# Kernel optimization log

Hardware: AMD Instinct MI355X
Metric: run time of the kernel (lower is better)

The kernel has to match this reference:

```python
import jax, jax.numpy as jnp
import numpy as np

PC_RANGE = [-51.2, -51.2, -5.0, 51.2, 51.2, 3.0]
VOXEL = [0.1, 0.1, 0.2]
OSF = 8
NUM_PRIOR = 100
C = 256
BN_EPS = 1e-5
LN_EPS = 1e-5


def _conv(x, w, pad):
    # x: [B,C,H,W], w: [O,I,kh,kw]
    return jax.lax.conv_general_dilated(
        x, w, window_strides=(1, 1), padding=[(pad, pad), (pad, pad)],
        dimension_numbers=('NCHW', 'OIHW', 'NCHW'))


def _bn(x, g, b, m, v):
    scale = (g / jnp.sqrt(v + BN_EPS))[None, :, None, None]
    return (x - m[None, :, None, None]) * scale + b[None, :, None, None]


def setup_inputs() -> dict:
    key = jax.random.key(0)
    ks = jax.random.split(key, 24)
    s3 = 1.0 / np.sqrt(C * 9)
    s1 = 1.0 / np.sqrt(C)
    inp = {
        'bev_feat': jax.random.normal(ks[0], (4, C, 128, 128), jnp.float32),
        'template_anchor': jax.random.normal(ks[1], (4, 900, 11), jnp.float32),
        # shared_conv: 3x3 conv (no bias) + BN(eval) + ReLU
        'shared_w': jax.random.normal(ks[2], (C, C, 3, 3), jnp.float32) * s3,
        'bn1_g': jax.random.normal(ks[3], (C,), jnp.float32) * 0.1 + 1.0,
        'bn1_b': jax.random.normal(ks[4], (C,), jnp.float32) * 0.1,
        'bn1_m': jax.random.normal(ks[5], (C,), jnp.float32) * 0.1,
        'bn1_v': jax.random.uniform(ks[6], (C,), jnp.float32) + 0.5,
        # objectness: 3x3 conv (no bias) + BN + ReLU + 1x1 conv (bias=-2)
        'obj_w1': jax.random.normal(ks[7], (C, C, 3, 3), jnp.float32) * s3,
        'bn2_g': jax.random.normal(ks[8], (C,), jnp.float32) * 0.1 + 1.0,
        'bn2_b': jax.random.normal(ks[9], (C,), jnp.float32) * 0.1,
        'bn2_m': jax.random.normal(ks[10], (C,), jnp.float32) * 0.1,
        'bn2_v': jax.random.uniform(ks[11], (C,), jnp.float32) + 0.5,
        'obj_w2': jax.random.normal(ks[12], (1, C, 1, 1), jnp.float32) * s1,
        'obj_b2': jnp.full((1,), -2.0, jnp.float32),
        # feat_proj: Linear + LN + ReLU + Linear
        'fp_w1': jax.random.normal(ks[13], (C, C), jnp.float32) * s1,
        'fp_b1': jax.random.normal(ks[14], (C,), jnp.float32) * 0.01,
        'ln_g': jnp.ones((C,), jnp.float32),
        'ln_b': jnp.zeros((C,), jnp.float32),
        'fp_w2': jax.random.normal(ks[15], (C, C), jnp.float32) * s1,
        'fp_b2': jax.random.normal(ks[16], (C,), jnp.float32) * 0.01,
        # geometry heads (1x1 convs, bias init 0)
        'z_w': jax.random.normal(ks[17], (1, C, 1, 1), jnp.float32) * s1,
        'z_b': jnp.zeros((1,), jnp.float32),
        'dim_w': jax.random.normal(ks[18], (3, C, 1, 1), jnp.float32) * s1,
        'dim_b': jnp.zeros((3,), jnp.float32),
        'yaw_w': jax.random.normal(ks[19], (2, C, 1, 1), jnp.float32) * s1,
        'yaw_b': jnp.zeros((2,), jnp.float32),
        'vel_w': jax.random.normal(ks[20], (2, C, 1, 1), jnp.float32) * s1,
        'vel_b': jnp.zeros((2,), jnp.float32),
    }
    return inp


def _forward(bev_feat, template_anchor, shared_w, bn1_g, bn1_b, bn1_m, bn1_v,
             obj_w1, bn2_g, bn2_b, bn2_m, bn2_v, obj_w2, obj_b2,
             fp_w1, fp_b1, ln_g, ln_b, fp_w2, fp_b2,
             z_w, z_b, dim_w, dim_b, yaw_w, yaw_b, vel_w, vel_b):
    B, Cc, H, W = bev_feat.shape
    # shared_conv
    feat = jax.nn.relu(_bn(_conv(bev_feat, shared_w, 1), bn1_g, bn1_b, bn1_m, bn1_v))
    # objectness heatmap
    h = jax.nn.relu(_bn(_conv(feat, obj_w1, 1), bn2_g, bn2_b, bn2_m, bn2_v))
    heatmap = jax.nn.sigmoid(_conv(h, obj_w2, 0) + obj_b2[None, :, None, None])
    score = heatmap.reshape(B, H * W)
    K = min(NUM_PRIOR, H * W, template_anchor.shape[1])
    topk_score, topk_inds = jax.lax.top_k(score, K)  # [B,K]
    ys = topk_inds // W
    xs = topk_inds % W
    # gather BEV features at topk locations: [B,K,C]
    feat_flat = feat.reshape(B, Cc, H * W).transpose(0, 2, 1)
    gathered = jnp.take_along_axis(feat_flat, topk_inds[:, :, None], axis=1)
    # feat_proj: Linear + LN + ReLU + Linear
    x = gathered @ fp_w1.T + fp_b1
    mu = jnp.mean(x, axis=-1, keepdims=True)
    var = jnp.mean((x - mu) ** 2, axis=-1, keepdims=True)
    x = (x - mu) / jnp.sqrt(var + LN_EPS) * ln_g + ln_b
    x = jax.nn.relu(x)
    prior_feature = x @ fp_w2.T + fp_b2
    prior_feature = prior_feature * (1.0 + topk_score[:, :, None])
    # geometry heads (1x1 convs == linear on gathered features)
    z_pred = gathered @ z_w[:, :, 0, 0].T + z_b      # [B,K,1]
    dim_pred = gathered @ dim_w[:, :, 0, 0].T + dim_b  # [B,K,3]
    yaw_pred = gathered @ yaw_w[:, :, 0, 0].T + yaw_b  # [B,K,2]
    vel_pred = gathered @ vel_w[:, :, 0, 0].T + vel_b  # [B,K,2]
    # anchor update
    pa = template_anchor[:, :K, :]
    x_metric = (xs.astype(pa.dtype) + 0.5) * (VOXEL[0] * OSF) + PC_RANGE[0]
    y_metric = (ys.astype(pa.dtype) + 0.5) * (VOXEL[1] * OSF) + PC_RANGE[1]
    z_new = pa[..., 2] + 0.5 * z_pred[..., 0]
    dims_new = pa[..., 3:6] + 0.2 * jnp.clip(dim_pred, -1.0, 1.0)
    yaw = jnp.tanh(yaw_pred)
    nrm = jnp.maximum(jnp.sqrt(jnp.sum(yaw * yaw, axis=-1, keepdims=True)), 1e-6)
    yaw_new = 0.7 * pa[..., 6:8] + 0.3 * (yaw / nrm)
    vel_new = pa[..., 8:10] + 0.2 * jnp.clip(vel_pred, -2.0, 2.0)
    prior_anchor = jnp.concatenate([
        x_metric[..., None], y_metric[..., None], z_new[..., None],
        dims_new, yaw_new, vel_new, pa[..., 10:]], axis=-1)
    return prior_feature, prior_anchor, topk_score


def reference(bev_feat, template_anchor, shared_w, bn1_g, bn1_b, bn1_m, bn1_v,
              obj_w1, bn2_g, bn2_b, bn2_m, bn2_v, obj_w2, obj_b2,
              fp_w1, fp_b1, ln_g, ln_b, fp_w2, fp_b2,
              z_w, z_b, dim_w, dim_b, yaw_w, yaw_b, vel_w, vel_b):
    return _forward(bev_feat, template_anchor, shared_w, bn1_g, bn1_b, bn1_m, bn1_v,
                    obj_w1, bn2_g, bn2_b, bn2_m, bn2_v, obj_w2, obj_b2,
                    fp_w1, fp_b1, ln_g, ln_b, fp_w2, fp_b2,
                    z_w, z_b, dim_w, dim_b, yaw_w, yaw_b, vel_w, vel_b)
```

## Files before the change

### kernel.cpp

```cpp
#include <hip/hip_runtime.h>
#include <math.h>


typedef __attribute__((ext_vector_type(8))) short bf16x8;
typedef __attribute__((ext_vector_type(4))) float f32x4;

#define HW 16384
#define WPITCH 130
#define CCAP 192
#define PSTR 28
#define WSO_XN    0ULL
#define WSO_FEATB 34078720ULL
#define WSO_WP1   68157440ULL
#define WSO_WP2   69337088ULL
#define WSO_BNP   70516736ULL
#define WSO_LOG   70521856ULL
#define WSO_CAND  70784000ULL
#define WSO_CNT   70787072ULL
#define WSO_EXL   70787136ULL
#define WSO_TIDX  70790208ULL
#define WSO_TLOG  70791808ULL
#define WSO_W1N   70793408ULL
#define WSO_W2N   73152704ULL
#define WSO_PBUF  WSO_XN

__device__ __forceinline__ float bf2f(short s) {
  return __uint_as_float(((unsigned)(unsigned short)s) << 16);
}
__device__ __forceinline__ short f2bf(float f) {
  unsigned u = __float_as_uint(f);
  u += 0x7fffu + ((u >> 16) & 1u);
  return (short)(u >> 16);
}
__device__ __forceinline__ void gll16(const void* g, void* l) {
  __builtin_amdgcn_global_load_lds(
      (const __attribute__((address_space(1))) void*)g,
      (__attribute__((address_space(3))) void*)l, 16, 0, 0);
}

__global__ void wprep(const float* __restrict__ src, short* __restrict__ wp,
                      float* __restrict__ wn) {
  int i = blockIdx.x * 256 + threadIdx.x;
  float v = src[i];
  int k = i % 9;
  int r = i / 9;
  int ci = r & 255;
  int co = r >> 8;
  wp[(k * 256 + co) * 256 + ci] = f2bf(v);
  wn[(ci * 9 + k) * 256 + co] = v;
}

__global__ void bnprep(const float* g1, const float* b1, const float* m1,
                       const float* v1, const float* g2, const float* b2,
                       const float* m2, const float* v2, const float* w2,
                       float* __restrict__ out) {
  int c = threadIdx.x;
  float s1 = g1[c] / sqrtf(v1[c] + 1e-5f);
  out[c] = s1;
  out[256 + c] = b1[c] - m1[c] * s1;
  float s2 = g2[c] / sqrtf(v2[c] + 1e-5f);
  out[512 + c] = s2;
  out[768 + c] = b2[c] - m2[c] * s2;
  out[1024 + c] = w2[c];
}

__global__ void padzero(short* __restrict__ xn, short* __restrict__ featb) {
  int i = blockIdx.x * 256 + threadIdx.x;
  int c = i & 255;
  int r = i >> 8;
  int nh = r >> 1;
  int side = r & 1;
  size_t off = ((size_t)nh * WPITCH + (side ? 129 : 0)) * 256 + c;
  xn[off] = 0;
  featb[off] = 0;
}

__global__ void loginit(float* __restrict__ logits, const float* __restrict__ b2) {
  logits[blockIdx.x * 256 + threadIdx.x] = b2[0];
}

__global__ __launch_bounds__(256) void nchw2nhwc(const float* __restrict__ in,
                                                 short* __restrict__ out) {
  __shared__ short tl[64 * 66];
  int n = blockIdx.z, c0 = blockIdx.y * 64, s0 = blockIdx.x * 64;
  int sl = threadIdx.x & 63, cl = threadIdx.x >> 6;
  for (int p = 0; p < 16; ++p) {
    int c = cl + p * 4;
    tl[c * 66 + sl] = f2bf(in[(((size_t)(n * 256 + c0 + c)) << 14) + s0 + sl]);
  }
  __syncthreads();
  int co = threadIdx.x & 63, so = threadIdx.x >> 6;
  for (int p = 0; p < 16; ++p) {
    int S = s0 + so + p * 4;
    int h = S >> 7, w = S & 127;
    out[(((size_t)(n * 128 + h)) * WPITCH + w + 1) * 256 + c0 + co] =
        tl[co * 66 + (so + p * 4)];
  }
}

template <int OUT_LOGITS>
__global__ __launch_bounds__(256) void conv3x3(const short* __restrict__ inp,
                                               const short* __restrict__ wp,
                                               const float* __restrict__ scale,
                                               const float* __restrict__ shift,
                                               const float* __restrict__ w2f,
                                               short* __restrict__ outb,
                                               float* __restrict__ logits) {
  __shared__ short a_sm[3][128 * 32];
  __shared__ short b_sm[3][128 * 32];
  const int t = threadIdx.x;
  const int wv = t >> 6, lane = t & 63;
  const int l15 = lane & 15, quad = lane >> 4;
  const int tile = blockIdx.x;
  const int img = tile >> 7;
  const int h = tile & 127;
  const int nblk = blockIdx.y;
  const int m0 = (wv & 1) << 6;
  const int n0 = (wv >> 1) << 6;

  f32x4 acc[4][4];
#pragma unroll
  for (int i = 0; i < 4; ++i)
#pragma unroll
    for (int j = 0; j < 4; ++j) {
      acc[i][j][0] = 0.f; acc[i][j][1] = 0.f;
      acc[i][j][2] = 0.f; acc[i][j][3] = 0.f;
    }

  for (int dhi = 0; dhi < 3; ++dhi) {
    const int hy = h + dhi - 1;
    if (hy < 0 || hy > 127) continue;
    const size_t arow = ((size_t)(img * 128 + hy)) * WPITCH;
    const short* wbase = wp + ((size_t)(dhi * 3 * 256 + nblk * 128)) * 256;

    for (int c0 = 0; c0 < 256; c0 += 32) {
      __syncthreads();
#pragma unroll
      for (int dwi = 0; dwi < 3; ++dwi) {
#pragma unroll
        for (int j = 0; j < 2; ++j) {
          const int mrow = (j << 6) + (t >> 2);
          const int cc = t & 3;
          gll16(inp + (arow + mrow + dwi) * 256 + c0 + cc * 8,
                a_sm[dwi] + ((size_t)((j << 8) + t)) * 8);
        }
      }
#pragma unroll
      for (int dwi = 0; dwi < 3; ++dwi) {
        const short* wtap = wbase + (size_t)dwi * 65536;
#pragma unroll
        for (int j = 0; j < 2; ++j) {
          const int nrow = (j << 6) + (t >> 2);
          const int cc = t & 3;
          gll16(wtap + (size_t)nrow * 256 + c0 + cc * 8,
                b_sm[dwi] + ((size_t)((j << 8) + t)) * 8);
        }
      }
      __syncthreads();

#pragma unroll
      for (int dwi = 0; dwi < 3; ++dwi) {
        bf16x8 af[4], bfr[4];
#pragma unroll
        for (int i = 0; i < 4; ++i)
          af[i] = *(const bf16x8*)(a_sm[dwi] + (m0 + i * 16 + l15) * 32 + quad * 8);
#pragma unroll
        for (int i = 0; i < 4; ++i)
          bfr[i] = *(const bf16x8*)(b_sm[dwi] + (n0 + i * 16 + l15) * 32 + quad * 8);
#pragma unroll
        for (int i = 0; i < 4; ++i)
#pragma unroll
          for (int j = 0; j < 4; ++j)
            acc[i][j] = __builtin_amdgcn_mfma_f32_16x16x32_bf16(af[i], bfr[j],
                                                                acc[i][j], 0, 0, 0);
      }
    }
  }

  float sc[4], sh[4], wf[4];
#pragma unroll
  for (int j = 0; j < 4; ++j) {
    const int co = nblk * 128 + n0 + j * 16 + l15;
    sc[j] = scale[co];
    sh[j] = shift[co];
    if (OUT_LOGITS) wf[j] = w2f[co];
  }
  if (OUT_LOGITS) {
    float* lrow = logits + ((size_t)img << 14) + (h << 7);
#pragma unroll
    for (int i = 0; i < 4; ++i) {
#pragma unroll
      for (int r = 0; r < 4; ++r) {
        float part = 0.f;
#pragma unroll
        for (int j = 0; j < 4; ++j) {
          float v = fmaxf(acc[i][j][r] * sc[j] + sh[j], 0.f);
          part += v * wf[j];
        }
        part += __shfl_xor(part, 1);
        part += __shfl_xor(part, 2);
        part += __shfl_xor(part, 4);
        part += __shfl_xor(part, 8);
        if (l15 == 0)
          atomicAdd(&lrow[m0 + i * 16 + quad * 4 + r], part);
      }
    }
  } else {
    const size_t obase = ((size_t)(img * 128 + h)) * WPITCH + 1;
#pragma unroll
    for (int i = 0; i < 4; ++i) {
#pragma unroll
      for (int j = 0; j < 4; ++j) {
        const int co = nblk * 128 + n0 + j * 16 + l15;
#pragma unroll
        for (int r = 0; r < 4; ++r) {
          const int m = m0 + i * 16 + quad * 4 + r;
          float v = fmaxf(acc[i][j][r] * sc[j] + sh[j], 0.f);
          outb[(obase + m) * 256 + co] = f2bf(v);
        }
      }
    }
  }
}

__global__ __launch_bounds__(1024) void topk_radix(const float* __restrict__ logits,
                                                   int* __restrict__ cand,
                                                   int* __restrict__ cnt_out) {
  __shared__ int hist[2048];
  __shared__ int wsum[16];
  __shared__ unsigned sel_bin;
  __shared__ int sel_above;
  __shared__ int cntr;
  const int b = blockIdx.x, t = threadIdx.x;
  const int lane = t & 63, wid = t >> 6;
  const float* L = logits + (size_t)b * HW;
  const int base = t * 16;
  unsigned kv[16];
#pragma unroll
  for (int i = 0; i < 4; ++i) {
    float4 v = *(const float4*)(L + base + i * 4);
    float f4[4] = {v.x, v.y, v.z, v.w};
#pragma unroll
    for (int j = 0; j < 4; ++j) {
      unsigned u = __float_as_uint(f4[j]);
      kv[i * 4 + j] = u ^ (((unsigned)((int)u >> 31)) | 0x80000000u);
    }
  }
  unsigned prefix = 0, pmask = 0;
  int need = 128;
  const int shifts[3] = {21, 10, 0};
  const int nbs[3] = {2048, 2048, 1024};

  for (int lev = 0; lev < 3; ++lev) {
    const int shift = shifts[lev];
    const int nb = nbs[lev];
    hist[t] = 0;
    hist[t + 1024] = 0;
    __syncthreads();
#pragma unroll
    for (int i = 0; i < 16; ++i)
      if ((kv[i] & pmask) == prefix)
        atomicAdd(&hist[(kv[i] >> shift) & (nb - 1)], 1);
    __syncthreads();
    const int cs = nb >> 10;
    const int bin_hi = nb - 1 - t * cs;
    const int c_hi = hist[bin_hi];
    const int c_lo = (cs == 2) ? hist[bin_hi - 1] : 0;
    const int s = c_hi + c_lo;
    int inc = s;
    for (int off = 1; off < 64; off <<= 1) {
      int nbr = __shfl_up(inc, off);
      if (lane >= off) inc += nbr;
    }
    if (lane == 63) wsum[wid] = inc;
    __syncthreads();
    if (wid == 0) {
      int wv = (lane < 16) ? wsum[lane] : 0;
      for (int off = 1; off < 16; off <<= 1) {
        int nbr = __shfl_up(wv, off);
        if (lane >= off) wv += nbr;
      }
      if (lane < 16) wsum[lane] = wv;
    }
    __syncthreads();
    const int excl = inc - s + (wid ? wsum[wid - 1] : 0);
    if (excl < need && need <= excl + s) {
      if (need <= excl + c_hi) {
        sel_bin = (unsigned)bin_hi;
        sel_above = excl;
      } else {
        sel_bin = (unsigned)(bin_hi - 1);
        sel_above = excl + c_hi;
      }
    }
    __syncthreads();
    prefix |= sel_bin << shift;
    pmask |= ((unsigned)(nb - 1)) << shift;
    need -= sel_above;
    __syncthreads();
  }
  if (t == 0) cntr = 0;
  __syncthreads();
#pragma unroll
  for (int i = 0; i < 16; ++i) {
    if (kv[i] >= prefix) {
      int p = atomicAdd(&cntr, 1);
      if (p < CCAP) cand[b * CCAP + p] = base + i;
    }
  }
  __syncthreads();
  if (t == 0) cnt_out[b] = (cntr < CCAP) ? cntr : CCAP;
}

__global__ __launch_bounds__(256) void patchstage(const float* __restrict__ x,
                                                  const int* __restrict__ cand,
                                                  const int* __restrict__ cnt,
                                                  float* __restrict__ pbuf) {
  const int c = blockIdx.x, b = blockIdx.y, t = threadIdx.x;
  if (c >= cnt[b]) return;
  const int s = cand[b * CCAP + c];
  const int h0 = (s >> 7) - 2, w0 = (s & 127) - 2;
  const float* xb = x + ((size_t)b << 22);
  float* pc = pbuf + (size_t)(b * CCAP + c) * (256 * PSTR);
#pragma unroll
  for (int k = 0; k < 25; ++k) {
    int e = t + (k << 8);
    int ci = e / 25;
    int rj = e - ci * 25;
    int r = rj / 5;
    int j = rj - r * 5;
    int hy = h0 + r, wx = w0 + j;
    float v = 0.f;
    if (hy >= 0 && hy < 128 && wx >= 0 && wx < 128)
      v = xb[((size_t)ci << 14) + (hy << 7) + wx];
    pc[ci * PSTR + rj] = v;
  }
}

__global__ __launch_bounds__(1024) void rescore(const float* __restrict__ pbuf,
                                                const float* __restrict__ w1n,
                                                const float* __restrict__ w2n,
                                                const float* __restrict__ bnp,
                                                const float* __restrict__ b2,
                                                const int* __restrict__ cand,
                                                const int* __restrict__ cnt,
                                                float* __restrict__ exlog) {
  const int bx = blockIdx.x, b = blockIdx.y, t = threadIdx.x;
  const int n = cnt[b];
  const int co = t & 255;
  const int ks = __builtin_amdgcn_readfirstlane(t >> 8);
  const int ci0 = ks << 6;
  __shared__ float a1pA[4 * 256 * 9];
  __shared__ float a1pB[4 * 256 * 9];
  __shared__ float f9A[256 * 12];
  __shared__ float f9B[256 * 12];
  __shared__ float accA_p[4 * 256];
  __shared__ float accB_p[4 * 256];
  __shared__ float redA[4], redB[4];

  for (int pass = 0; pass < 2; ++pass) {
    const int c0 = bx + (pass ? 128 : 0);
    if (c0 >= n) break;
    const int c1 = bx + 64;
    const bool hasB = (pass == 0);
    if (pass) __syncthreads();

    const float* ppA = pbuf + ((size_t)(b * CCAP + c0)) * (256 * PSTR);
    const float* ppB = pbuf + ((size_t)(b * CCAP + (hasB ? c1 : c0))) * (256 * PSTR);

    float aA[9], aB[9];
#pragma unroll
    for (int p = 0; p < 9; ++p) { aA[p] = 0.f; aB[p] = 0.f; }
    for (int ci = ci0; ci < ci0 + 64; ++ci) {
      const float* wr = w1n + (size_t)ci * 2304 + co;
      float w9[9];
#pragma unroll
      for (int k = 0; k < 9; ++k) w9[k] = wr[k * 256];
      {
        const float* pc = ppA + ci * PSTR;
        float xp[25];
#pragma unroll
        for (int p = 0; p < 25; ++p) xp[p] = pc[p];
#pragma unroll
        for (int py = 0; py < 3; ++py)
#pragma unroll
          for (int px = 0; px < 3; ++px)
#pragma unroll
            for (int ky = 0; ky < 3; ++ky)
#pragma unroll
              for (int kx = 0; kx < 3; ++kx)
                aA[py * 3 + px] += w9[ky * 3 + kx] * xp[(py + ky) * 5 + px + kx];
      }
      if (hasB) {
        const float* pc = ppB + ci * PSTR;
        float xp[25];
#pragma unroll
        for (int p = 0; p < 25; ++p) xp[p] = pc[p];
#pragma unroll
        for (int py = 0; py < 3; ++py)
#pragma unroll
          for (int px = 0; px < 3; ++px)
#pragma unroll
            for (int ky = 0; ky < 3; ++ky)
#pragma unroll
              for (int kx = 0; kx < 3; ++kx)
                aB[py * 3 + px] += w9[ky * 3 + kx] * xp[(py + ky) * 5 + px + kx];
      }
    }
#pragma unroll
    for (int p = 0; p < 9; ++p) {
      a1pA[(ks * 256 + co) * 9 + p] = aA[p];
      if (hasB) a1pB[(ks * 256 + co) * 9 + p] = aB[p];
    }
    __syncthreads();

    if (t < 256) {
      const float sc1 = bnp[t], sh1 = bnp[256 + t];
#pragma unroll
      for (int p = 0; p < 9; ++p) {
        float vA = a1pA[t * 9 + p] + a1pA[(256 + t) * 9 + p] +
                   a1pA[(512 + t) * 9 + p] + a1pA[(768 + t) * 9 + p];
        f9A[t * 12 + p] = fmaxf(vA * sc1 + sh1, 0.f);
        if (hasB) {
          float vB = a1pB[t * 9 + p] + a1pB[(256 + t) * 9 + p] +
                     a1pB[(512 + t) * 9 + p] + a1pB[(768 + t) * 9 + p];
          f9B[t * 12 + p] = fmaxf(vB * sc1 + sh1, 0.f);
        }
      }
    }
    __syncthreads();

    float accA = 0.f, accB = 0.f;
    for (int ci = ci0; ci < ci0 + 64; ++ci) {
      const float* wr = w2n + (size_t)ci * 2304 + co;
      float w9[9];
#pragma unroll
      for (int k = 0; k < 9; ++k) w9[k] = wr[k * 256];
      {
        float f9[12];
        const float4* fr = (const float4*)(f9A + ci * 12);
#pragma unroll
        for (int q = 0; q < 3; ++q) {
          float4 v = fr[q];
          f9[q * 4 + 0] = v.x; f9[q * 4 + 1] = v.y;
          f9[q * 4 + 2] = v.z; f9[q * 4 + 3] = v.w;
        }
#pragma unroll
        for (int k = 0; k < 9; ++k) accA += w9[k] * f9[k];
      }
      if (hasB) {
        float f9[12];
        const float4* fr = (const float4*)(f9B + ci * 12);
#pragma unroll
        for (int q = 0; q < 3; ++q) {
          float4 v = fr[q];
          f9[q * 4 + 0] = v.x; f9[q * 4 + 1] = v.y;
          f9[q * 4 + 2] = v.z; f9[q * 4 + 3] = v.w;
        }
#pragma unroll
        for (int k = 0; k < 9; ++k) accB += w9[k] * f9[k];
      }
    }
    accA_p[ks * 256 + co] = accA;
    if (hasB) accB_p[ks * 256 + co] = accB;
    __syncthreads();

    if (t < 256) {
      const float sc2 = bnp[512 + t], sh2 = bnp[768 + t], wf = bnp[1024 + t];
      float a = accA_p[t] + accA_p[256 + t] + accA_p[512 + t] + accA_p[768 + t];
      float pA = fmaxf(a * sc2 + sh2, 0.f) * wf;
      float pB = 0.f;
      if (hasB) {
        float bb = accB_p[t] + accB_p[256 + t] + accB_p[512 + t] + accB_p[768 + t];
        pB = fmaxf(bb * sc2 + sh2, 0.f) * wf;
      }
      for (int off = 32; off; off >>= 1) {
        pA += __shfl_xor(pA, off);
        pB += __shfl_xor(pB, off);
      }
      if ((t & 63) == 0) {
        redA[t >> 6] = pA;
        redB[t >> 6] = pB;
      }
    }
    __syncthreads();
    if (t == 0) {
      exlog[b * CCAP + c0] = redA[0] + redA[1] + redA[2] + redA[3] + b2[0];
      if (hasB)
        exlog[b * CCAP + c1] = redB[0] + redB[1] + redB[2] + redB[3] + b2[0];
    }
  }
}

__global__ __launch_bounds__(CCAP) void final_topk(const float* __restrict__ exlog,
                                                   const int* __restrict__ cand,
                                                   const int* __restrict__ cnt,
                                                   int* __restrict__ tidx,
                                                   float* __restrict__ tlog) {
  const int b = blockIdx.x, t = threadIdx.x;
  __shared__ float v[CCAP];
  __shared__ int si[CCAP];
  const int n = cnt[b];
  float mv = (t < n) ? exlog[b * CCAP + t] : -3.0e38f;
  int s = (t < n) ? cand[b * CCAP + t] : 0x7FFFFFFF;
  v[t] = mv;
  si[t] = s;
  __syncthreads();
  int rank = 0;
  for (int j = 0; j < CCAP; ++j) {
    float vj = v[j];
    int sj = si[j];
    if (vj > mv || (vj == mv && sj < s)) ++rank;
  }
  if (t < n && rank < 100) {
    tidx[b * 100 + rank] = s;
    tlog[b * 100 + rank] = mv;
  }
}

__global__ __launch_bounds__(256) void head_kern(
    const short* __restrict__ featb, const int* __restrict__ tidx,
    const float* __restrict__ tlog, const float* __restrict__ tmpl,
    const float* __restrict__ w1, const float* __restrict__ b1,
    const float* __restrict__ lng, const float* __restrict__ lnb,
    const float* __restrict__ w2, const float* __restrict__ b2,
    const float* __restrict__ zw, const float* __restrict__ zb,
    const float* __restrict__ dmw, const float* __restrict__ dmb,
    const float* __restrict__ yw, const float* __restrict__ yb,
    const float* __restrict__ vw, const float* __restrict__ vb,
    float* __restrict__ out) {
  const int blk = blockIdx.x;
  const int b = blk / 100, q = blk % 100;
  const int t = threadIdx.x;
  const int lane = t & 63, wid = t >> 6;
  __shared__ float g[256];
  __shared__ float sx[256];
  __shared__ float red[4];
  __shared__ float heads[8];

  const int s = tidx[b * 100 + q];
  const float score = 1.f / (1.f + expf(-tlog[b * 100 + q]));
  const int ys = s >> 7, xs = s & 127;

  g[t] = bf2f(featb[(((size_t)(b * 128 + ys)) * WPITCH + xs + 1) * 256 + t]);
  __syncthreads();

  float x = b1[t];
  {
    const float* wr = w1 + (size_t)t * 256;
    for (int i = 0; i < 256; i += 4) {
      float4 wv = *(const float4*)(wr + i);
      x += g[i] * wv.x + g[i + 1] * wv.y + g[i + 2] * wv.z + g[i + 3] * wv.w;
    }
  }
  float sum = x;
  for (int off = 32; off; off >>= 1) sum += __shfl_xor(sum, off);
  if (lane == 0) red[wid] = sum;
  __syncthreads();
  float mu = (red[0] + red[1] + red[2] + red[3]) * (1.f / 256.f);
  __syncthreads();
  float d = x - mu;
  float q2 = d * d;
  for (int off = 32; off; off >>= 1) q2 += __shfl_xor(q2, off);
  if (lane == 0) red[wid] = q2;
  __syncthreads();
  float var = (red[0] + red[1] + red[2] + red[3]) * (1.f / 256.f);
  float xn = d * (1.f / sqrtf(var + 1e-5f)) * lng[t] + lnb[t];
  xn = fmaxf(xn, 0.f);
  sx[t] = xn;
  __syncthreads();
  float pf = b2[t];
  {
    const float* wr = w2 + (size_t)t * 256;
    for (int i = 0; i < 256; i += 4) {
      float4 wv = *(const float4*)(wr + i);
      pf += sx[i] * wv.x + sx[i + 1] * wv.y + sx[i + 2] * wv.z + sx[i + 3] * wv.w;
    }
  }
  pf *= (1.f + score);
  out[(size_t)(b * 100 + q) * 256 + t] = pf;

  const int k = t >> 5, l = t & 31;
  const float* hw;
  float hb;
  if (k == 0)      { hw = zw;                 hb = zb[0]; }
  else if (k < 4)  { hw = dmw + (k - 1) * 256; hb = dmb[k - 1]; }
  else if (k < 6)  { hw = yw + (k - 4) * 256;  hb = yb[k - 4]; }
  else             { hw = vw + (k - 6) * 256;  hb = vb[k - 6]; }
  float hp = 0.f;
#pragma unroll
  for (int r = 0; r < 8; ++r) {
    int i = l + r * 32;
    hp += g[i] * hw[i];
  }
  for (int off = 16; off; off >>= 1) hp += __shfl_xor(hp, off);
  if (l == 0) heads[k] = hp + hb;
  __syncthreads();

  if (t == 0) {
    const float* pa = tmpl + ((size_t)b * 900 + q) * 11;
    float p[11];
#pragma unroll
    for (int i = 0; i < 11; ++i) p[i] = pa[i];
    float a[11];
    a[0] = ((float)xs + 0.5f) * 0.8f - 51.2f;
    a[1] = ((float)ys + 0.5f) * 0.8f - 51.2f;
    a[2] = p[2] + 0.5f * heads[0];
#pragma unroll
    for (int i = 0; i < 3; ++i)
      a[3 + i] = p[3 + i] + 0.2f * fminf(fmaxf(heads[1 + i], -1.f), 1.f);
    float t0 = tanhf(heads[4]), t1 = tanhf(heads[5]);
    float nrm = fmaxf(sqrtf(t0 * t0 + t1 * t1), 1e-6f);
    a[6] = 0.7f * p[6] + 0.3f * t0 / nrm;
    a[7] = 0.7f * p[7] + 0.3f * t1 / nrm;
    a[8] = p[8] + 0.2f * fminf(fmaxf(heads[6], -2.f), 2.f);
    a[9] = p[9] + 0.2f * fminf(fmaxf(heads[7], -2.f), 2.f);
    a[10] = p[10];
    float* oa = out + 102400 + (size_t)(b * 100 + q) * 11;
#pragma unroll
    for (int i = 0; i < 11; ++i) oa[i] = a[i];
    out[106800 + b * 100 + q] = score;
  }
}

extern "C" void kernel_launch(void* const* d_in, const int* in_sizes, int n_in,
                              void* d_out, int out_size, void* d_ws, size_t ws_size,
                              hipStream_t stream) {
  (void)in_sizes; (void)n_in; (void)out_size; (void)ws_size;
  char* ws = (char*)d_ws;
  short* xn     = (short*)(ws + WSO_XN);
  short* featb  = (short*)(ws + WSO_FEATB);
  short* wp1    = (short*)(ws + WSO_WP1);
  short* wp2    = (short*)(ws + WSO_WP2);
  float* bnp    = (float*)(ws + WSO_BNP);
  float* logits = (float*)(ws + WSO_LOG);
  int*   cand   = (int*)(ws + WSO_CAND);
  int*   cnt    = (int*)(ws + WSO_CNT);
  float* exl    = (float*)(ws + WSO_EXL);
  int*   tidx   = (int*)(ws + WSO_TIDX);
  float* tlog   = (float*)(ws + WSO_TLOG);
  float* w1n    = (float*)(ws + WSO_W1N);
  float* w2n    = (float*)(ws + WSO_W2N);
  float* pbuf   = (float*)(ws + WSO_PBUF);

  const float* bev = (const float*)d_in[0];

  wprep<<<2304, 256, 0, stream>>>((const float*)d_in[2], wp1, w1n);
  wprep<<<2304, 256, 0, stream>>>((const float*)d_in[7], wp2, w2n);
  bnprep<<<1, 256, 0, stream>>>(
      (const float*)d_in[3], (const float*)d_in[4], (const float*)d_in[5],
      (const float*)d_in[6], (const float*)d_in[8], (const float*)d_in[9],
      (const float*)d_in[10], (const float*)d_in[11], (const float*)d_in[12], bnp);
  padzero<<<1024, 256, 0, stream>>>(xn, featb);
  loginit<<<256, 256, 0, stream>>>(logits, (const float*)d_in[13]);
  nchw2nhwc<<<dim3(256, 4, 4), 256, 0, stream>>>(bev, xn);
  conv3x3<0><<<dim3(512, 2), 256, 0, stream>>>(xn, wp1, bnp, bnp + 256,
                                               nullptr, featb, nullptr);
  conv3x3<1><<<dim3(512, 2), 256, 0, stream>>>(featb, wp2, bnp + 512, bnp + 768,
                                               bnp + 1024, nullptr, logits);
  topk_radix<<<4, 1024, 0, stream>>>(logits, cand, cnt);
  patchstage<<<dim3(CCAP, 4), 256, 0, stream>>>(bev, cand, cnt, pbuf);
  rescore<<<dim3(64, 4), 1024, 0, stream>>>(pbuf, w1n, w2n, bnp,
                                            (const float*)d_in[13], cand, cnt,
                                            exl);
  final_topk<<<4, CCAP, 0, stream>>>(exl, cand, cnt, tidx, tlog);
  head_kern<<<400, 256, 0, stream>>>(
      featb, tidx, tlog, (const float*)d_in[1],
      (const float*)d_in[14], (const float*)d_in[15], (const float*)d_in[16],
      (const float*)d_in[17], (const float*)d_in[18], (const float*)d_in[19],
      (const float*)d_in[20], (const float*)d_in[21], (const float*)d_in[22],
      (const float*)d_in[23], (const float*)d_in[24], (const float*)d_in[25],
      (const float*)d_in[26], (const float*)d_in[27], (float*)d_out);
}
```

Before: 546.0 us.

## Share one haloed input row tile across conv taps and merge prep kernels

```diff
diff --git a/kernel.cpp b/kernel.cpp
--- a/kernel.cpp
+++ b/kernel.cpp
@@ -38,9 +38,19 @@
       (__attribute__((address_space(3))) void*)l, 16, 0, 0);
 }
 
-__global__ void wprep(const float* __restrict__ src, short* __restrict__ wp,
-                      float* __restrict__ wn) {
-  int i = blockIdx.x * 256 + threadIdx.x;
+__global__ void wprep2(const float* __restrict__ s1, const float* __restrict__ s2,
+                       short* __restrict__ wp1, short* __restrict__ wp2,
+                       float* __restrict__ wn1, float* __restrict__ wn2) {
+  int bx = blockIdx.x;
+  const float* src;
+  short* wp;
+  float* wn;
+  if (bx >= 2304) {
+    src = s2; wp = wp2; wn = wn2; bx -= 2304;
+  } else {
+    src = s1; wp = wp1; wn = wn1;
+  }
+  int i = bx * 256 + threadIdx.x;
   float v = src[i];
   int k = i % 9;
   int r = i / 9;
@@ -50,33 +60,33 @@
   wn[(ci * 9 + k) * 256 + co] = v;
 }
 
-__global__ void bnprep(const float* g1, const float* b1, const float* m1,
-                       const float* v1, const float* g2, const float* b2,
-                       const float* m2, const float* v2, const float* w2,
-                       float* __restrict__ out) {
-  int c = threadIdx.x;
-  float s1 = g1[c] / sqrtf(v1[c] + 1e-5f);
-  out[c] = s1;
-  out[256 + c] = b1[c] - m1[c] * s1;
-  float s2 = g2[c] / sqrtf(v2[c] + 1e-5f);
-  out[512 + c] = s2;
-  out[768 + c] = b2[c] - m2[c] * s2;
-  out[1024 + c] = w2[c];
-}
-
-__global__ void padzero(short* __restrict__ xn, short* __restrict__ featb) {
-  int i = blockIdx.x * 256 + threadIdx.x;
-  int c = i & 255;
-  int r = i >> 8;
-  int nh = r >> 1;
-  int side = r & 1;
-  size_t off = ((size_t)nh * WPITCH + (side ? 129 : 0)) * 256 + c;
-  xn[off] = 0;
-  featb[off] = 0;
-}
-
-__global__ void loginit(float* __restrict__ logits, const float* __restrict__ b2) {
-  logits[blockIdx.x * 256 + threadIdx.x] = b2[0];
+__global__ void smallprep(const float* g1, const float* b1, const float* m1,
+                          const float* v1, const float* g2, const float* b2,
+                          const float* m2, const float* v2, const float* w2,
+                          const float* ob2, float* __restrict__ bnp,
+                          short* __restrict__ xn, short* __restrict__ featb,
+                          float* __restrict__ logits) {
+  const int blk = blockIdx.x, t = threadIdx.x;
+  if (blk < 1024) {
+    int i = blk * 256 + t;
+    int c = i & 255;
+    int r = i >> 8;
+    int nh = r >> 1;
+    int side = r & 1;
+    size_t off = ((size_t)nh * WPITCH + (side ? 129 : 0)) * 256 + c;
+    xn[off] = 0;
+    featb[off] = 0;
+  } else if (blk < 1280) {
+    logits[(blk - 1024) * 256 + t] = ob2[0];
+  } else {
+    float s1 = g1[t] / sqrtf(v1[t] + 1e-5f);
+    bnp[t] = s1;
+    bnp[256 + t] = b1[t] - m1[t] * s1;
+    float s2 = g2[t] / sqrtf(v2[t] + 1e-5f);
+    bnp[512 + t] = s2;
+    bnp[768 + t] = b2[t] - m2[t] * s2;
+    bnp[1024 + t] = w2[t];
+  }
 }
 
 __global__ __launch_bounds__(256) void nchw2nhwc(const float* __restrict__ in,
@@ -106,7 +116,7 @@
                                                const float* __restrict__ w2f,
                                                short* __restrict__ outb,
                                                float* __restrict__ logits) {
-  __shared__ short a_sm[3][128 * 32];
+  __shared__ short a_sm[132 * 32];
   __shared__ short b_sm[3][128 * 32];
   const int t = threadIdx.x;
   const int wv = t >> 6, lane = t & 63;
@@ -136,14 +146,16 @@
     for (int c0 = 0; c0 < 256; c0 += 32) {
       __syncthreads();
 #pragma unroll
-      for (int dwi = 0; dwi < 3; ++dwi) {
-#pragma unroll
-        for (int j = 0; j < 2; ++j) {
-          const int mrow = (j << 6) + (t >> 2);
-          const int cc = t & 3;
-          gll16(inp + (arow + mrow + dwi) * 256 + c0 + cc * 8,
-                a_sm[dwi] + ((size_t)((j << 8) + t)) * 8);
-        }
+      for (int j = 0; j < 2; ++j) {
+        const int seg = (j << 6) + (t >> 2);
+        const int cc = t & 3;
+        gll16(inp + (arow + seg) * 256 + c0 + cc * 8,
+              a_sm + ((size_t)((j << 8) + t)) * 8);
+      }
+      if (t < 32) {
+        const int r = t >> 4, dw = t & 15;
+        const int* gsrc = (const int*)(inp + (arow + 128 + r) * 256 + c0) + dw;
+        ((int*)a_sm)[(128 + r) * 16 + dw] = *gsrc;
       }
 #pragma unroll
       for (int dwi = 0; dwi < 3; ++dwi) {
@@ -163,7 +175,7 @@
         bf16x8 af[4], bfr[4];
 #pragma unroll
         for (int i = 0; i < 4; ++i)
-          af[i] = *(const bf16x8*)(a_sm[dwi] + (m0 + i * 16 + l15) * 32 + quad * 8);
+          af[i] = *(const bf16x8*)(a_sm + (dwi + m0 + i * 16 + l15) * 32 + quad * 8);
 #pragma unroll
         for (int i = 0; i < 4; ++i)
           bfr[i] = *(const bf16x8*)(b_sm[dwi] + (n0 + i * 16 + l15) * 32 + quad * 8);
@@ -645,14 +657,13 @@
 
   const float* bev = (const float*)d_in[0];
 
-  wprep<<<2304, 256, 0, stream>>>((const float*)d_in[2], wp1, w1n);
-  wprep<<<2304, 256, 0, stream>>>((const float*)d_in[7], wp2, w2n);
-  bnprep<<<1, 256, 0, stream>>>(
+  wprep2<<<4608, 256, 0, stream>>>((const float*)d_in[2], (const float*)d_in[7],
+                                   wp1, wp2, w1n, w2n);
+  smallprep<<<1281, 256, 0, stream>>>(
       (const float*)d_in[3], (const float*)d_in[4], (const float*)d_in[5],
       (const float*)d_in[6], (const float*)d_in[8], (const float*)d_in[9],
-      (const float*)d_in[10], (const float*)d_in[11], (const float*)d_in[12], bnp);
-  padzero<<<1024, 256, 0, stream>>>(xn, featb);
-  loginit<<<256, 256, 0, stream>>>(logits, (const float*)d_in[13]);
+      (const float*)d_in[10], (const float*)d_in[11], (const float*)d_in[12],
+      (const float*)d_in[13], bnp, xn, featb, logits);
   nchw2nhwc<<<dim3(256, 4, 4), 256, 0, stream>>>(bev, xn);
   conv3x3<0><<<dim3(512, 2), 256, 0, stream>>>(xn, wp1, bnp, bnp + 256,
                                                nullptr, featb, nullptr);
```

After: 540.0 us. No clear change (-1.1%).
